# Kernel tuning notes

Measured on AMD Instinct MI355X. Metric: run time of the kernel, lower is better.

## Reference

```python
import jax, jax.numpy as jnp
import numpy as np

G = 2            # num codevector groups
C = 320          # codes per group
VQ_DIM = 256     # codevector_dim
D = VQ_DIM // G  # per-group code dim = 128
TAU = 2.0        # gumbel temperature


def setup_inputs() -> dict:
    key = jax.random.key(0)
    k1, k2, k3, k4, k5, k6 = jax.random.split(key, 6)
    B, T, H = 16, 3072, 512
    x = jax.random.normal(k1, (B, T, H), dtype=jnp.float32)
    masked_token_idx = jax.random.randint(k2, (B, T), 0, 2) > 0  # bool mask
    gumbel_noise = jax.random.gumbel(k3, (B * T * G, C), dtype=jnp.float32)
    q_proj_w = jax.random.normal(k4, (G * C, H), dtype=jnp.float32) * (1.0 / np.sqrt(H))
    q_proj_b = jax.random.normal(k5, (G * C,), dtype=jnp.float32) * 0.02
    codevectors = jax.random.uniform(k6, (1, G * C, D), dtype=jnp.float32)
    return {"x": x, "masked_token_idx": masked_token_idx, "gumbel_noise": gumbel_noise,
            "q_proj_w": q_proj_w, "q_proj_b": q_proj_b, "codevectors": codevectors}


def _perplexity(probs, mask_flat):
    # probs: [B*T, G, C]; masked mean over tokens, then per-codebook perplexity
    m = mask_flat.astype(probs.dtype)
    denom = jnp.maximum(m.sum(), 1.0)
    p = jnp.einsum('ngc,n->gc', probs, m) / denom  # [G, C]
    perp_per_cb = jnp.exp(-jnp.sum(p * jnp.log(p + 1e-7), axis=-1))
    return perp_per_cb.sum()


def reference(x, masked_token_idx, gumbel_noise, q_proj_w, q_proj_b, codevectors):
    B, T, H = x.shape
    N = B * T
    logits = jnp.einsum('bth,kh->btk', x, q_proj_w) + q_proj_b  # [B,T,G*C]
    l = logits.reshape(N * G, C)
    # hard gumbel-softmax with straight-through estimator (training path)
    y_soft = jax.nn.softmax((l + gumbel_noise) / TAU, axis=-1)
    idx = jnp.argmax(y_soft, axis=-1)
    y_hard = jax.nn.one_hot(idx, C, dtype=y_soft.dtype)
    codevector_probs = y_hard + y_soft - jax.lax.stop_gradient(y_soft)  # [N*G, C]
    # perplexity from plain (non-tempered) softmax of logits, over masked tokens
    soft = jax.nn.softmax(l.reshape(N, G, C), axis=-1)
    perplexity = _perplexity(soft, masked_token_idx.reshape(-1))
    # codevector gather-multiply-sum, expressed as a grouped contraction
    # (same math as probs.unsqueeze(-1)*codevectors then sum over codes)
    cv = codevectors.reshape(G, C, D)
    probs3 = codevector_probs.reshape(N, G, C)
    selected = jnp.einsum('ngc,gcd->ngd', probs3, cv).reshape(B, T, G * D)
    return selected, perplexity
```

## Files before the change

kernel.cpp:

```cpp
#include <hip/hip_runtime.h>
#include <hip/hip_bf16.h>
#include <math.h>

#define TOKS 49152
#define HD   512
#define GN   2
#define CN   320
#define DN   128
#define BM   64
#define NTHR 512
#define LSTR 321
#define ASTR 36
#define SB_L 20480
#define SA   40960
#define SMEM_SZ 51328

#define BMF  32
#define NTHRF 256
#define WSTR 33

#define WS_WELEMS ((size_t)(GN * CN) * HD)
#define WS_W_OFF  4096
#define WS_MID    (WS_W_OFF + 4 * WS_WELEMS)

typedef _Float16 f16x8 __attribute__((ext_vector_type(8)));
typedef float    fx4   __attribute__((ext_vector_type(4)));

#define GLD_LDS16(gp, lp)                                                    \
  __builtin_amdgcn_global_load_lds(                                          \
      (const __attribute__((address_space(1))) void*)(gp),                   \
      (__attribute__((address_space(3))) void*)(lp), 16, 0, 0)

#define CVT8(U, V, HH, LL) do {                                              \
    _Pragma("unroll")                                                        \
    for (int e = 0; e < 4; ++e) {                                            \
      _Float16 h;                                                            \
      h = (_Float16)U[e]; HH[e] = h;                                         \
      LL[e] = (_Float16)((U[e] - (float)h) * 512.f);                         \
      h = (_Float16)V[e]; HH[e + 4] = h;                                     \
      LL[e + 4] = (_Float16)((V[e] - (float)h) * 512.f);                     \
    }                                                                        \
  } while (0)

__global__ void k_zero(float* pp) {
  int t = threadIdx.x;
  if (t < GN * CN) pp[t] = 0.f;
}

__global__ __launch_bounds__(256) void k_split(const float* __restrict__ src,
                                               _Float16* __restrict__ dh,
                                               _Float16* __restrict__ dl,
                                               float* __restrict__ pp) {
  if (blockIdx.x < 3) {
    int i = blockIdx.x * 256 + threadIdx.x;
    if (i < GN * CN) pp[i] = 0.f;
  }
  size_t t    = (size_t)blockIdx.x * 256 + threadIdx.x;
  int    lane = (int)(t & 63);
  size_t blob = t >> 6;
  int    k0   = (int)(blob & 15);
  size_t rb   = blob >> 4;
  const float* p = src + (rb * 16 + (lane & 15)) * HD + k0 * 32 + (lane >> 4) * 8;
  fx4 u = *(const fx4*)p;
  fx4 v = *(const fx4*)(p + 4);
  f16x8 h8, l8;
  #pragma unroll
  for (int e = 0; e < 4; ++e) {
    _Float16 hu = (_Float16)u[e], hv = (_Float16)v[e];
    h8[e]     = hu;
    h8[e + 4] = hv;
    l8[e]     = (_Float16)((u[e] - (float)hu) * 512.f);
    l8[e + 4] = (_Float16)((v[e] - (float)hv) * 512.f);
  }
  *(f16x8*)(dh + t * 8) = h8;
  *(f16x8*)(dl + t * 8) = l8;
}

__global__ __launch_bounds__(NTHR, 4) void k_gemm_ep(
    const float* __restrict__ x, const int* __restrict__ mask,
    const float* __restrict__ gnoise, const float* __restrict__ bias,
    const float* __restrict__ cv, const _Float16* __restrict__ wh,
    const _Float16* __restrict__ wl, float* __restrict__ out,
    float* __restrict__ pp)
{
  __shared__ __align__(16) char smem[SMEM_SZ];
  float* As   = (float*)(smem + SA);
  float* lg   = (float*)smem;
  float* psum = (float*)(smem + 41088);

  const int u   = blockIdx.x;
  const int mt  = ((u >> 4) << 3) | (u & 7);
  const int g   = (u >> 3) & 1;
  const int m0  = mt * BM;
  const int tid = threadIdx.x;
  const int tc  = tid & 63;
  const int w   = tid >> 6;
  const int wr  = w >> 2;
  const int wc  = w & 3;
  const int l15 = tid & 15;
  const int l4  = tc >> 4;

  fx4 aH[2][5], aL[2][5];
  #pragma unroll
  for (int rf = 0; rf < 2; ++rf)
    #pragma unroll
    for (int cf = 0; cf < 5; ++cf) {
      aH[rf][cf] = (fx4){0.f, 0.f, 0.f, 0.f};
      aL[rf][cf] = (fx4){0.f, 0.f, 0.f, 0.f};
    }

  const _Float16* bb = (w < 4) ? wh : wl;
  const int cb0      = (w < 4) ? w * 5 : w * 5 - 20;
  const _Float16* bsrc = bb + (size_t)(g * 20 + cb0) * 8192 + (size_t)tc * 8;
  char* bdst = smem + (size_t)(w * 5) * 1024;
  const int ar = w * 8 + (tc >> 3);
  const int ac = tc & 7;
  const float* asrc = x + (size_t)(m0 + ar) * HD + ac * 4;
  float* adst = &As[ar * ASTR + ac * 4];

  #pragma unroll 1
  for (int t = 0; t < 16; ++t) {
    __syncthreads();
    fx4 av = *(const fx4*)(asrc + t * 32);
    #pragma unroll
    for (int q = 0; q < 5; ++q)
      GLD_LDS16(bsrc + (size_t)q * 8192 + (size_t)t * 512, bdst + q * 1024);
    *(fx4*)adst = av;
    __syncthreads();

    const float* a0p = &As[(wr * 32 + l15) * ASTR + l4 * 8];
    fx4 u0 = *(const fx4*)a0p;
    fx4 v0 = *(const fx4*)(a0p + 4);
    fx4 u1 = *(const fx4*)(a0p + 16 * ASTR);
    fx4 v1 = *(const fx4*)(a0p + 16 * ASTR + 4);
    f16x8 A0h, A0l, A1h, A1l;
    CVT8(u0, v0, A0h, A0l);
    CVT8(u1, v1, A1h, A1l);
    #pragma unroll
    for (int cf = 0; cf < 5; ++cf) {
      f16x8 Bh = *(const f16x8*)(smem + (wc * 5 + cf) * 1024 + tc * 16);
      f16x8 Bl = *(const f16x8*)(smem + SB_L + (wc * 5 + cf) * 1024 + tc * 16);
      aH[0][cf] = __builtin_amdgcn_mfma_f32_16x16x32_f16(A0h, Bh, aH[0][cf], 0, 0, 0);
      aH[1][cf] = __builtin_amdgcn_mfma_f32_16x16x32_f16(A1h, Bh, aH[1][cf], 0, 0, 0);
      aL[0][cf] = __builtin_amdgcn_mfma_f32_16x16x32_f16(A0h, Bl, aL[0][cf], 0, 0, 0);
      aL[0][cf] = __builtin_amdgcn_mfma_f32_16x16x32_f16(A0l, Bh, aL[0][cf], 0, 0, 0);
      aL[1][cf] = __builtin_amdgcn_mfma_f32_16x16x32_f16(A1h, Bl, aL[1][cf], 0, 0, 0);
      aL[1][cf] = __builtin_amdgcn_mfma_f32_16x16x32_f16(A1l, Bh, aL[1][cf], 0, 0, 0);
    }
  }
  __syncthreads();

  float bj[5];
  #pragma unroll
  for (int cf = 0; cf < 5; ++cf) bj[cf] = bias[g * CN + wc * 80 + cf * 16 + l15];

  float pacc[5] = {0.f, 0.f, 0.f, 0.f, 0.f};
  #pragma unroll
  for (int p = 0; p < 2; ++p) {
    if (wr == p) {
      #pragma unroll
      for (int cf = 0; cf < 5; ++cf) {
        const int col = wc * 80 + cf * 16 + l15;
        #pragma unroll
        for (int rf = 0; rf < 2; ++rf)
          #pragma unroll
          for (int e = 0; e < 4; ++e)
            lg[(rf * 16 + l4 * 4 + e) * LSTR + col] =
                aH[rf][cf][e] + aL[rf][cf][e] * (1.f / 512.f) + bj[cf];
      }
    }
    __syncthreads();
    #pragma unroll
    for (int i = 0; i < 4; ++i) {
      const int rl = w * 4 + i;
      const int n  = m0 + p * 32 + rl;
      const size_t grow = ((size_t)n * GN + g) * CN;
      float lv[5], gv[5];
      #pragma unroll
      for (int j = 0; j < 5; ++j) lv[j] = lg[rl * LSTR + tc + 64 * j];
      #pragma unroll
      for (int j = 0; j < 5; ++j) gv[j] = gnoise[grow + tc + 64 * j];

      float bv = -3.4e38f; int bi = 1 << 30;
      #pragma unroll
      for (int j = 0; j < 5; ++j) {
        float v = lv[j] + gv[j];
        if (v > bv) { bv = v; bi = tc + 64 * j; }
      }
      for (int off = 1; off < 64; off <<= 1) {
        float ov = __shfl_xor(bv, off);
        int   oi = __shfl_xor(bi, off);
        if (ov > bv || (ov == bv && oi < bi)) { bv = ov; bi = oi; }
      }

      float mx = lv[0];
      #pragma unroll
      for (int j = 1; j < 5; ++j) mx = fmaxf(mx, lv[j]);
      for (int off = 1; off < 64; off <<= 1) mx = fmaxf(mx, __shfl_xor(mx, off));
      float e[5], s = 0.f;
      #pragma unroll
      for (int j = 0; j < 5; ++j) { e[j] = __expf(lv[j] - mx); s += e[j]; }
      for (int off = 1; off < 64; off <<= 1) s += __shfl_xor(s, off);
      const float inv = 1.f / s;
      const float mlt = (mask[n] != 0) ? 1.f : 0.f;
      #pragma unroll
      for (int j = 0; j < 5; ++j) pacc[j] += mlt * e[j] * inv;

      const float2* cvr = (const float2*)(cv + ((size_t)(g * CN + bi)) * DN);
      float2* o2 = (float2*)(out + (size_t)n * (GN * DN) + g * DN);
      o2[tc] = cvr[tc];
    }
    __syncthreads();
  }

  #pragma unroll
  for (int j = 0; j < 5; ++j) psum[w * CN + tc + 64 * j] = pacc[j];
  __syncthreads();
  for (int c = tid; c < CN; c += NTHR) {
    float s = 0.f;
    #pragma unroll
    for (int q = 0; q < 8; ++q) s += psum[q * CN + c];
    atomicAdd(&pp[g * CN + c], s);
  }
}

__global__ __launch_bounds__(NTHRF) void k_main_fp32(
    const float* __restrict__ x, const int* __restrict__ mask,
    const float* __restrict__ gnoise, const float* __restrict__ W,
    const float* __restrict__ bias, const float* __restrict__ cv,
    float* __restrict__ out, float* __restrict__ pp)
{
  __shared__ __align__(16) char smem[47360];
  float* w_lds = (float*)smem;
  float* xs    = (float*)(smem + 42240);
  float* lg    = (float*)smem;
  float* psum  = (float*)(smem + 42240);

  const int m0  = blockIdx.x * BMF;
  const int g   = blockIdx.y;
  const int tid = threadIdx.x;
  const int tc  = tid & 63;
  const int tr  = tid >> 6;
  const int r0  = tr * 8;

  float acc[8][5];
  #pragma unroll
  for (int i = 0; i < 8; ++i)
    #pragma unroll
    for (int j = 0; j < 5; ++j) acc[i][j] = 0.f;

  const float* Wg = W + (size_t)g * CN * HD;

  for (int k0 = 0; k0 < HD; k0 += 32) {
    __syncthreads();
    #pragma unroll
    for (int t = 0; t < 10; ++t) {
      int idx = tid + t * NTHRF;
      int c   = idx >> 3;
      int k4  = idx & 7;
      float4 wv4 = *(const float4*)(Wg + (size_t)c * HD + k0 + k4 * 4);
      float* dst = &w_lds[c * WSTR + k4 * 4];
      dst[0] = wv4.x; dst[1] = wv4.y; dst[2] = wv4.z; dst[3] = wv4.w;
    }
    {
      int r = tid >> 3, k4 = tid & 7;
      float4 xv = *(const float4*)(x + (size_t)(m0 + r) * HD + k0 + k4 * 4);
      float* dst = &xs[r * 32 + k4 * 4];
      dst[0] = xv.x; dst[1] = xv.y; dst[2] = xv.z; dst[3] = xv.w;
    }
    __syncthreads();
    #pragma unroll
    for (int kk = 0; kk < 32; kk += 4) {
      float xq[8][4];
      #pragma unroll
      for (int i = 0; i < 8; ++i) {
        float4 t4 = *(const float4*)&xs[(r0 + i) * 32 + kk];
        xq[i][0] = t4.x; xq[i][1] = t4.y; xq[i][2] = t4.z; xq[i][3] = t4.w;
      }
      #pragma unroll
      for (int q = 0; q < 4; ++q) {
        float wv[5];
        #pragma unroll
        for (int j = 0; j < 5; ++j) wv[j] = w_lds[(tc + 64 * j) * WSTR + kk + q];
        #pragma unroll
        for (int i = 0; i < 8; ++i)
          #pragma unroll
          for (int j = 0; j < 5; ++j)
            acc[i][j] = fmaf(xq[i][q], wv[j], acc[i][j]);
      }
    }
  }
  __syncthreads();

  float bj[5];
  #pragma unroll
  for (int j = 0; j < 5; ++j) bj[j] = bias[g * CN + tc + 64 * j];
  #pragma unroll
  for (int i = 0; i < 8; ++i)
    #pragma unroll
    for (int j = 0; j < 5; ++j)
      lg[(r0 + i) * CN + tc + 64 * j] = acc[i][j] + bj[j];
  __syncthreads();

  float pacc[5] = {0.f, 0.f, 0.f, 0.f, 0.f};
  #pragma unroll
  for (int i = 0; i < 8; ++i) {
    const int r = r0 + i;
    const int n = m0 + r;
    const size_t grow = ((size_t)n * GN + g) * CN;
    float lv[5], gv[5];
    #pragma unroll
    for (int j = 0; j < 5; ++j) lv[j] = lg[r * CN + tc + 64 * j];
    #pragma unroll
    for (int j = 0; j < 5; ++j) gv[j] = gnoise[grow + tc + 64 * j];

    float bv = -3.4e38f; int bi = 1 << 30;
    #pragma unroll
    for (int j = 0; j < 5; ++j) {
      float v = lv[j] + gv[j];
      if (v > bv) { bv = v; bi = tc + 64 * j; }
    }
    for (int off = 1; off < 64; off <<= 1) {
      float ov = __shfl_xor(bv, off);
      int   oi = __shfl_xor(bi, off);
      if (ov > bv || (ov == bv && oi < bi)) { bv = ov; bi = oi; }
    }

    float mx = lv[0];
    #pragma unroll
    for (int j = 1; j < 5; ++j) mx = fmaxf(mx, lv[j]);
    for (int off = 1; off < 64; off <<= 1) mx = fmaxf(mx, __shfl_xor(mx, off));
    float e[5], s = 0.f;
    #pragma unroll
    for (int j = 0; j < 5; ++j) { e[j] = expf(lv[j] - mx); s += e[j]; }
    for (int off = 1; off < 64; off <<= 1) s += __shfl_xor(s, off);
    const float inv = 1.f / s;
    const float mlt = (mask[n] != 0) ? 1.f : 0.f;
    #pragma unroll
    for (int j = 0; j < 5; ++j) pacc[j] += mlt * e[j] * inv;

    const float2* cvr = (const float2*)(cv + ((size_t)(g * CN + bi)) * DN);
    float2* o2 = (float2*)(out + (size_t)n * (GN * DN) + g * DN);
    o2[tc] = cvr[tc];
  }

  #pragma unroll
  for (int j = 0; j < 5; ++j) psum[tr * CN + tc + 64 * j] = pacc[j];
  __syncthreads();
  for (int c = tid; c < CN; c += NTHRF) {
    float s = psum[c] + psum[CN + c] + psum[2 * CN + c] + psum[3 * CN + c];
    atomicAdd(&pp[g * CN + c], s);
  }
}

__global__ __launch_bounds__(640) void k_final(
    const float* __restrict__ pp, const int* __restrict__ mask,
    float* __restrict__ out, int out_off)
{
  __shared__ float red[10];
  __shared__ float eL[GN * CN];
  __shared__ float perp_parts[GN];
  const int tid = threadIdx.x;

  float cnt = 0.f;
  for (int i = tid; i < TOKS; i += 640) cnt += (mask[i] != 0) ? 1.f : 0.f;
  for (int off = 1; off < 64; off <<= 1) cnt += __shfl_xor(cnt, off);
  if ((tid & 63) == 0) red[tid >> 6] = cnt;
  __syncthreads();
  float denom = 0.f;
  #pragma unroll
  for (int w = 0; w < 10; ++w) denom += red[w];
  denom = fmaxf(denom, 1.f);

  const float p = pp[tid] / denom;
  eL[tid] = p * logf(p + 1e-7f);
  __syncthreads();

  if (tid < 2 * 64) {
    const int gg = tid >> 6, ll = tid & 63;
    float s = 0.f;
    #pragma unroll
    for (int j = 0; j < 5; ++j) s += eL[gg * CN + ll + 64 * j];
    for (int off = 1; off < 64; off <<= 1) s += __shfl_xor(s, off);
    if (ll == 0) perp_parts[gg] = expf(-s);
  }
  __syncthreads();
  if (tid == 0) out[out_off] = perp_parts[0] + perp_parts[1];
}

extern "C" void kernel_launch(void* const* d_in, const int* in_sizes, int n_in,
                              void* d_out, int out_size, void* d_ws, size_t ws_size,
                              hipStream_t stream) {
  const float* x     = (const float*)d_in[0];
  const int*   mask  = (const int*)d_in[1];
  const float* gn    = (const float*)d_in[2];
  const float* W     = (const float*)d_in[3];
  const float* bias  = (const float*)d_in[4];
  const float* cv    = (const float*)d_in[5];
  float* out = (float*)d_out;
  float* pp  = (float*)d_ws;

  if (ws_size >= WS_MID) {
    _Float16* wh = (_Float16*)((char*)d_ws + WS_W_OFF);
    _Float16* wl = wh + WS_WELEMS;
    hipLaunchKernelGGL(k_split, dim3((int)(WS_WELEMS / 8 / 256)), dim3(256), 0,
                       stream, W, wh, wl, pp);
    hipLaunchKernelGGL(k_gemm_ep, dim3(TOKS / BM * GN), dim3(NTHR), 0, stream,
                       x, mask, gn, bias, cv, wh, wl, out, pp);
  } else {
    hipLaunchKernelGGL(k_zero, dim3(1), dim3(640), 0, stream, pp);
    hipLaunchKernelGGL(k_main_fp32, dim3(TOKS / BMF, GN), dim3(NTHRF), 0, stream,
                       x, mask, gn, W, bias, cv, out, pp);
  }

  hipLaunchKernelGGL(k_final, dim3(1), dim3(640), 0, stream,
                     pp, mask, out, out_size - 1);
}
```

Measured before the change: 208.2 us.

## Double-buffer GEMM LDS stages and pre-split A tile into fp16 hi/lo

The GEMM main loop now double-buffers its shared-memory tiles, so the next K-slice of weights and activations is fetched while the current one feeds the MFMAs. This removes one of the two barriers per iteration. The activation tile is converted to fp16 hi/lo once at staging time and stored in MFMA fragment layout, instead of every wave re-converting fp32 rows after reading them. The cost is 96KB of dynamic LDS per block and launch bounds lowered from 4 to 2 blocks per CU, which cuts occupancy. The epilogue logits stride also changes.

```diff
diff --git a/kernel.cpp b/kernel.cpp
--- a/kernel.cpp
+++ b/kernel.cpp
@@ -9,11 +9,15 @@
 #define DN   128
 #define BM   64
 #define NTHR 512
-#define LSTR 321
-#define ASTR 36
-#define SB_L 20480
-#define SA   40960
-#define SMEM_SZ 51328
+#define LSTR 324
+
+#define BH_OFF 0
+#define BL_OFF 20480
+#define AH_OFF 40960
+#define AL_OFF 45056
+#define SBUF   49152
+#define SMEM_DYN (2 * SBUF)
+#define PSUM_OFF 41472
 
 #define BMF  32
 #define NTHRF 256
@@ -30,17 +34,6 @@
   __builtin_amdgcn_global_load_lds(                                          \
       (const __attribute__((address_space(1))) void*)(gp),                   \
       (__attribute__((address_space(3))) void*)(lp), 16, 0, 0)
-
-#define CVT8(U, V, HH, LL) do {                                              \
-    _Pragma("unroll")                                                        \
-    for (int e = 0; e < 4; ++e) {                                            \
-      _Float16 h;                                                            \
-      h = (_Float16)U[e]; HH[e] = h;                                         \
-      LL[e] = (_Float16)((U[e] - (float)h) * 512.f);                         \
-      h = (_Float16)V[e]; HH[e + 4] = h;                                     \
-      LL[e + 4] = (_Float16)((V[e] - (float)h) * 512.f);                     \
-    }                                                                        \
-  } while (0)
 
 __global__ void k_zero(float* pp) {
   int t = threadIdx.x;
@@ -76,17 +69,16 @@
   *(f16x8*)(dl + t * 8) = l8;
 }
 
-__global__ __launch_bounds__(NTHR, 4) void k_gemm_ep(
+__global__ __launch_bounds__(NTHR, 2) void k_gemm_ep(
     const float* __restrict__ x, const int* __restrict__ mask,
     const float* __restrict__ gnoise, const float* __restrict__ bias,
     const float* __restrict__ cv, const _Float16* __restrict__ wh,
     const _Float16* __restrict__ wl, float* __restrict__ out,
     float* __restrict__ pp)
 {
-  __shared__ __align__(16) char smem[SMEM_SZ];
-  float* As   = (float*)(smem + SA);
+  extern __shared__ __align__(16) char smem[];
   float* lg   = (float*)smem;
-  float* psum = (float*)(smem + 41088);
+  float* psum = (float*)(smem + PSUM_OFF);
 
   const int u   = blockIdx.x;
   const int mt  = ((u >> 4) << 3) | (u & 7);
@@ -112,43 +104,63 @@
   const _Float16* bb = (w < 4) ? wh : wl;
   const int cb0      = (w < 4) ? w * 5 : w * 5 - 20;
   const _Float16* bsrc = bb + (size_t)(g * 20 + cb0) * 8192 + (size_t)tc * 8;
-  char* bdst = smem + (size_t)(w * 5) * 1024;
-  const int ar = w * 8 + (tc >> 3);
-  const int ac = tc & 7;
-  const float* asrc = x + (size_t)(m0 + ar) * HD + ac * 4;
-  float* adst = &As[ar * ASTR + ac * 4];
-
-  #pragma unroll 1
+  const int arow = tid >> 2;
+  const int al4  = tid & 3;
+  const float* asrc = x + (size_t)(m0 + arow) * HD + al4 * 8;
+  const int aslot = (arow >> 4) * 1024 + ((arow & 15) + 16 * al4) * 16;
+
+#define STAGE(T, BASE) do {                                                  \
+    _Pragma("unroll")                                                        \
+    for (int q = 0; q < 5; ++q)                                              \
+      GLD_LDS16(bsrc + (size_t)q * 8192 + (size_t)(T) * 512,                 \
+                (BASE) + w * 5120 + q * 1024);                               \
+    if (tid < 256) {                                                         \
+      fx4 au = *(const fx4*)(asrc + (size_t)(T) * 32);                       \
+      fx4 av = *(const fx4*)(asrc + (size_t)(T) * 32 + 4);                   \
+      f16x8 h8, l8;                                                          \
+      _Pragma("unroll")                                                      \
+      for (int e = 0; e < 4; ++e) {                                          \
+        _Float16 hh;                                                         \
+        hh = (_Float16)au[e]; h8[e] = hh;                                    \
+        l8[e] = (_Float16)((au[e] - (float)hh) * 512.f);                     \
+        hh = (_Float16)av[e]; h8[e + 4] = hh;                                \
+        l8[e + 4] = (_Float16)((av[e] - (float)hh) * 512.f);                 \
+      }                                                                      \
+      *(f16x8*)((BASE) + AH_OFF + aslot) = h8;                               \
+      *(f16x8*)((BASE) + AL_OFF + aslot) = l8;                               \
+    }                                                                        \
+  } while (0)
+
+#define COMPUTE(BASE) do {                                                   \
+    f16x8 A0h = *(const f16x8*)((BASE) + AH_OFF + (wr * 2 + 0) * 1024 + tc * 16); \
+    f16x8 A1h = *(const f16x8*)((BASE) + AH_OFF + (wr * 2 + 1) * 1024 + tc * 16); \
+    f16x8 A0l = *(const f16x8*)((BASE) + AL_OFF + (wr * 2 + 0) * 1024 + tc * 16); \
+    f16x8 A1l = *(const f16x8*)((BASE) + AL_OFF + (wr * 2 + 1) * 1024 + tc * 16); \
+    _Pragma("unroll")                                                        \
+    for (int cf = 0; cf < 5; ++cf) {                                         \
+      f16x8 Bh = *(const f16x8*)((BASE) + BH_OFF + (wc * 5 + cf) * 1024 + tc * 16); \
+      f16x8 Bl = *(const f16x8*)((BASE) + BL_OFF + (wc * 5 + cf) * 1024 + tc * 16); \
+      aH[0][cf] = __builtin_amdgcn_mfma_f32_16x16x32_f16(A0h, Bh, aH[0][cf], 0, 0, 0); \
+      aH[1][cf] = __builtin_amdgcn_mfma_f32_16x16x32_f16(A1h, Bh, aH[1][cf], 0, 0, 0); \
+      aL[0][cf] = __builtin_amdgcn_mfma_f32_16x16x32_f16(A0h, Bl, aL[0][cf], 0, 0, 0); \
+      aL[0][cf] = __builtin_amdgcn_mfma_f32_16x16x32_f16(A0l, Bh, aL[0][cf], 0, 0, 0); \
+      aL[1][cf] = __builtin_amdgcn_mfma_f32_16x16x32_f16(A1h, Bl, aL[1][cf], 0, 0, 0); \
+      aL[1][cf] = __builtin_amdgcn_mfma_f32_16x16x32_f16(A1l, Bh, aL[1][cf], 0, 0, 0); \
+    }                                                                        \
+  } while (0)
+
+  STAGE(0, smem);
+  __syncthreads();
+  #pragma unroll 2
   for (int t = 0; t < 16; ++t) {
+    char* cur = smem + (size_t)(t & 1) * SBUF;
+    char* nxt = smem + (size_t)((t & 1) ^ 1) * SBUF;
+    if (t < 15) STAGE(t + 1, nxt);
+    COMPUTE(cur);
     __syncthreads();
-    fx4 av = *(const fx4*)(asrc + t * 32);
-    #pragma unroll
-    for (int q = 0; q < 5; ++q)
-      GLD_LDS16(bsrc + (size_t)q * 8192 + (size_t)t * 512, bdst + q * 1024);
-    *(fx4*)adst = av;
-    __syncthreads();
-
-    const float* a0p = &As[(wr * 32 + l15) * ASTR + l4 * 8];
-    fx4 u0 = *(const fx4*)a0p;
-    fx4 v0 = *(const fx4*)(a0p + 4);
-    fx4 u1 = *(const fx4*)(a0p + 16 * ASTR);
-    fx4 v1 = *(const fx4*)(a0p + 16 * ASTR + 4);
-    f16x8 A0h, A0l, A1h, A1l;
-    CVT8(u0, v0, A0h, A0l);
-    CVT8(u1, v1, A1h, A1l);
-    #pragma unroll
-    for (int cf = 0; cf < 5; ++cf) {
-      f16x8 Bh = *(const f16x8*)(smem + (wc * 5 + cf) * 1024 + tc * 16);
-      f16x8 Bl = *(const f16x8*)(smem + SB_L + (wc * 5 + cf) * 1024 + tc * 16);
-      aH[0][cf] = __builtin_amdgcn_mfma_f32_16x16x32_f16(A0h, Bh, aH[0][cf], 0, 0, 0);
-      aH[1][cf] = __builtin_amdgcn_mfma_f32_16x16x32_f16(A1h, Bh, aH[1][cf], 0, 0, 0);
-      aL[0][cf] = __builtin_amdgcn_mfma_f32_16x16x32_f16(A0h, Bl, aL[0][cf], 0, 0, 0);
-      aL[0][cf] = __builtin_amdgcn_mfma_f32_16x16x32_f16(A0l, Bh, aL[0][cf], 0, 0, 0);
-      aL[1][cf] = __builtin_amdgcn_mfma_f32_16x16x32_f16(A1h, Bl, aL[1][cf], 0, 0, 0);
-      aL[1][cf] = __builtin_amdgcn_mfma_f32_16x16x32_f16(A1l, Bh, aL[1][cf], 0, 0, 0);
-    }
-  }
-  __syncthreads();
+  }
+#undef STAGE
+#undef COMPUTE
 
   float bj[5];
   #pragma unroll
@@ -230,11 +242,11 @@
     const float* __restrict__ bias, const float* __restrict__ cv,
     float* __restrict__ out, float* __restrict__ pp)
 {
-  __shared__ __align__(16) char smem[47360];
-  float* w_lds = (float*)smem;
-  float* xs    = (float*)(smem + 42240);
-  float* lg    = (float*)smem;
-  float* psum  = (float*)(smem + 42240);
+  __shared__ __align__(16) char fsmem[47360];
+  float* w_lds = (float*)fsmem;
+  float* xs    = (float*)(fsmem + 42240);
+  float* lgf   = (float*)fsmem;
+  float* psum  = (float*)(fsmem + 42240);
 
   const int m0  = blockIdx.x * BMF;
   const int g   = blockIdx.y;
@@ -299,7 +311,7 @@
   for (int i = 0; i < 8; ++i)
     #pragma unroll
     for (int j = 0; j < 5; ++j)
-      lg[(r0 + i) * CN + tc + 64 * j] = acc[i][j] + bj[j];
+      lgf[(r0 + i) * CN + tc + 64 * j] = acc[i][j] + bj[j];
   __syncthreads();
 
   float pacc[5] = {0.f, 0.f, 0.f, 0.f, 0.f};
@@ -310,7 +322,7 @@
     const size_t grow = ((size_t)n * GN + g) * CN;
     float lv[5], gv[5];
     #pragma unroll
-    for (int j = 0; j < 5; ++j) lv[j] = lg[r * CN + tc + 64 * j];
+    for (int j = 0; j < 5; ++j) lv[j] = lgf[r * CN + tc + 64 * j];
     #pragma unroll
     for (int j = 0; j < 5; ++j) gv[j] = gnoise[grow + tc + 64 * j];
 
@@ -405,8 +417,8 @@
     _Float16* wl = wh + WS_WELEMS;
     hipLaunchKernelGGL(k_split, dim3((int)(WS_WELEMS / 8 / 256)), dim3(256), 0,
                        stream, W, wh, wl, pp);
-    hipLaunchKernelGGL(k_gemm_ep, dim3(TOKS / BM * GN), dim3(NTHR), 0, stream,
-                       x, mask, gn, bias, cv, wh, wl, out, pp);
+    hipLaunchKernelGGL(k_gemm_ep, dim3(TOKS / BM * GN), dim3(NTHR), SMEM_DYN,
+                       stream, x, mask, gn, bias, cv, wh, wl, out, pp);
   } else {
     hipLaunchKernelGGL(k_zero, dim3(1), dim3(640), 0, stream, pp);
     hipLaunchKernelGGL(k_main_fp32, dim3(TOKS / BMF, GN), dim3(NTHRF), 0, stream,
```

After: 231.2 us. +11.0%, slower.
